# Optimization experiments

Hardware: AMD Instinct MI355X
Metric: run time of the kernel (lower is better)

Reference implementation:

```python
import jax, jax.numpy as jnp
import numpy as np

N, E, D = 50000, 800000, 64  # nodes, edges, feature dim (all feature dims must match, see module)
EPS = 1e-5


def _linear_params(key, fin, fout):
    k1, k2 = jax.random.split(key)
    s = 1.0 / np.sqrt(fin)
    W = jax.random.uniform(k1, (fout, fin), minval=-s, maxval=s, dtype=jnp.float32)
    b = jax.random.uniform(k2, (fout,), minval=-s, maxval=s, dtype=jnp.float32)
    return W, b


def setup_inputs() -> dict:
    key = jax.random.key(0)
    ks = jax.random.split(key, 9)
    h = jax.random.normal(ks[0], (N, D), dtype=jnp.float32)
    e = jax.random.normal(ks[1], (E, D), dtype=jnp.float32)
    src = jax.random.randint(ks[2], (E,), 0, N)
    dst = jax.random.randint(ks[3], (E,), 0, N)
    W_upd, b_upd = _linear_params(ks[4], 3 * D, D)   # upd_linear: cat(h_src,h_dst,e) -> D
    W_act, b_act = _linear_params(ks[5], D, D)       # activation_linear
    W_gd, b_gd = _linear_params(ks[6], D, D)         # gating_dst_linear
    W_gs, b_gs = _linear_params(ks[7], D, D)         # gating_src_linear
    W_out, b_out = _linear_params(ks[8], D, D)       # final linear
    g_un = jnp.ones((D,), jnp.float32); be_un = jnp.zeros((D,), jnp.float32)  # upd_norm gamma/beta
    g_gn = jnp.ones((D,), jnp.float32); be_gn = jnp.zeros((D,), jnp.float32)  # gating_norm gamma/beta
    return dict(h=h, e=e, src=src, dst=dst,
                W_upd=W_upd, b_upd=b_upd, g_un=g_un, be_un=be_un,
                W_act=W_act, b_act=b_act, W_gd=W_gd, b_gd=b_gd,
                W_gs=W_gs, b_gs=b_gs, g_gn=g_gn, be_gn=be_gn,
                W_out=W_out, b_out=b_out)


def _batchnorm(x, gamma, beta):
    # nn.BatchNorm1d in training mode: biased batch stats over axis 0
    m = x.mean(axis=0)
    v = x.var(axis=0)
    return (x - m) * jax.lax.rsqrt(v + EPS) * gamma + beta


def reference(h, e, src, dst, W_upd, b_upd, g_un, be_un, W_act, b_act,
              W_gd, b_gd, W_gs, b_gs, g_gn, be_gn, W_out, b_out):
    n_nodes = h.shape[0]
    # --- edge update: gather endpoints, linear, batchnorm, SiLU, residual ---
    e_cat = jnp.concatenate([h[src], h[dst], e], axis=1)       # [E, 3D]
    e_lin = e_cat @ W_upd.T + b_upd                             # [E, D]
    e2 = e + jax.nn.silu(_batchnorm(e_lin, g_un, be_un))        # residual (dims equal)
    # --- edge softmax grouped by destination node ---
    logit = e2 @ W_act.T + b_act                                # [E, D]
    mx = jax.ops.segment_max(logit, dst, num_segments=n_nodes)  # [N, D]
    ex = jnp.exp(logit - mx[dst])
    den = jax.ops.segment_sum(ex, dst, num_segments=n_nodes)
    a = ex / den[dst]                                           # [E, D]
    # --- gated aggregation: mail = a * W_gd h_dst, scatter-sum to dst ---
    mail = a * (h[dst] @ W_gd.T + b_gd)                         # [E, D]
    agg = jax.ops.segment_sum(mail, dst, num_segments=n_nodes)  # [N, D]
    h2 = (h @ W_gs.T + b_gs) + agg
    h2 = jax.nn.silu(_batchnorm(h2, g_gn, be_gn)) + h
    h2 = h2 @ W_out.T + b_out
    return (h2, e2)
```

## Files before the change

kernel.cpp:

```cpp
#include <hip/hip_runtime.h>

#define N_NODES 50000
#define N_EDGES 800000
#define EPS_BN 1e-5f


typedef __attribute__((ext_vector_type(8))) short s16x8;
typedef __attribute__((ext_vector_type(4))) float f32x4;

__device__ __forceinline__ unsigned short f2bf(float f) {
  unsigned int u = __float_as_uint(f);
  u += 0x7FFFu + ((u >> 16) & 1u);
  return (unsigned short)(u >> 16);
}
__device__ __forceinline__ unsigned int pack2(float lo, float hi) {
  return (unsigned int)f2bf(lo) | ((unsigned int)f2bf(hi) << 16);
}
__device__ __forceinline__ s16x8 cvt8(float4 a, float4 b) {
  union { s16x8 v; unsigned int u[4]; } r;
  r.u[0] = pack2(a.x, a.y); r.u[1] = pack2(a.z, a.w);
  r.u[2] = pack2(b.x, b.y); r.u[3] = pack2(b.z, b.w);
  return r.v;
}
__device__ __forceinline__ float siluf(float x) { return x / (1.f + __expf(-x)); }

__global__ void k_pre(unsigned int* __restrict__ wsu,
                      const float* __restrict__ W_upd, const float* __restrict__ W_gd,
                      const float* __restrict__ W_gs, const float* __restrict__ W_out,
                      const float* __restrict__ h, short* __restrict__ hbf) {
  int b = blockIdx.x;
  if (b < 49) {
    int i = b * 256 + threadIdx.x;
    if (i < 512) wsu[i] = 0u;
    if (i < 12500) wsu[12800 + i] = 0u;
    if (i < 6144) {
      int s = i >> 2, w = i & 3;
      int row = s / 24, slot = s - row * 24;
      int ii = slot ^ (row & 7);
      int fidx = row * 192 + ii * 8 + w * 2;
      wsu[512 + i] = pack2(W_upd[fidx], W_upd[fidx + 1]);
    }
    if (i < 2048) {
      float2 a = *(const float2*)&W_gd[(size_t)i * 2];
      float2 bb = *(const float2*)&W_gs[(size_t)i * 2];
      float2 c = *(const float2*)&W_out[(size_t)i * 2];
      wsu[6656 + i] = pack2(a.x, a.y);
      wsu[8704 + i] = pack2(bb.x, bb.y);
      wsu[10752 + i] = pack2(c.x, c.y);
    }
  } else {
    int t = (b - 49) * 256 + threadIdx.x;
    if (t < (N_NODES * 64) / 8) {
      float4 a = *(const float4*)&h[(size_t)t * 8];
      float4 bb = *(const float4*)&h[(size_t)t * 8 + 4];
      *(s16x8*)&hbf[(size_t)t * 8] = cvt8(a, bb);
    }
  }
}

template<int PHASE>
__global__ __launch_bounds__(256, PHASE == 0 ? 5 : 4) void k_edge(
    const short* __restrict__ hbf, const float* __restrict__ e,
    const int* __restrict__ src, const int* __restrict__ dst,
    const unsigned int* __restrict__ wsu, const float* __restrict__ b_upd,
    const float* __restrict__ ws, unsigned char* __restrict__ flb,
    float* __restrict__ out_e)
{
  __shared__ short Bls[64 * 192];
  __shared__ float red[4][128];

  int tid = threadIdx.x;
  int ln = tid & 63, wv = tid >> 6;
  int lr = ln & 15, lq = ln >> 4, lk = lq * 8;
  int m0 = blockIdx.x * 128;
  int r0 = wv * 32 + lr, r1 = r0 + 16;
  int mA = m0 + r0, mB = m0 + r1;

  const float* pe0 = e + (size_t)mA * 64 + lk;
  const float* pe1 = e + (size_t)mB * 64 + lk;
  float4 e0a = *(const float4*)(pe0);
  float4 e0b = *(const float4*)(pe0 + 4);
  float4 e0c = *(const float4*)(pe0 + 32);
  float4 e0d = *(const float4*)(pe0 + 36);
  float4 e1a = *(const float4*)(pe1);
  float4 e1b = *(const float4*)(pe1 + 4);
  float4 e1c = *(const float4*)(pe1 + 32);
  float4 e1d = *(const float4*)(pe1 + 36);

  int s0 = src[mA], d0 = dst[mA];
  int s1i = src[mB], d1 = dst[mB];

  if (PHASE == 0 && lq == 0) { flb[d0] = 1; flb[d1] = 1; }

  s16x8 A0[6], A1[6];
  A0[0] = *(const s16x8*)&hbf[s0 * 64 + lk];
  A0[1] = *(const s16x8*)&hbf[s0 * 64 + 32 + lk];
  A0[2] = *(const s16x8*)&hbf[d0 * 64 + lk];
  A0[3] = *(const s16x8*)&hbf[d0 * 64 + 32 + lk];
  A1[0] = *(const s16x8*)&hbf[s1i * 64 + lk];
  A1[1] = *(const s16x8*)&hbf[s1i * 64 + 32 + lk];
  A1[2] = *(const s16x8*)&hbf[d1 * 64 + lk];
  A1[3] = *(const s16x8*)&hbf[d1 * 64 + 32 + lk];

  {
    unsigned int* bls32 = (unsigned int*)Bls;
    #pragma unroll
    for (int j = 0; j < 6; ++j) {
      int base = (j * 4 + wv) * 256;
      __builtin_amdgcn_global_load_lds(
          (__attribute__((address_space(1))) void*)(unsigned int*)(wsu + 512 + base + ln * 4),
          (__attribute__((address_space(3))) void*)(bls32 + base),
          16, 0, 0);
    }
  }

  A0[4] = cvt8(e0a, e0b);
  A0[5] = cvt8(e0c, e0d);
  A1[4] = cvt8(e1a, e1b);
  A1[5] = cvt8(e1c, e1d);
  __syncthreads();

  int rl = ln >> 4, c0 = (ln & 15) * 4;
  float4 epre[2][4];
  if (PHASE == 1) {
    #pragma unroll
    for (int rt = 0; rt < 2; ++rt)
      #pragma unroll
      for (int q = 0; q < 4; ++q)
        epre[rt][q] = *(const float4*)&e[(size_t)(m0 + wv * 32 + rt * 16 + rl * 4 + q) * 64 + c0];
  }

  f32x4 zero4 = {0.f, 0.f, 0.f, 0.f};
  f32x4 acc[2][4];
  #pragma unroll
  for (int rt = 0; rt < 2; ++rt)
    #pragma unroll
    for (int ct = 0; ct < 4; ++ct) acc[rt][ct] = zero4;

  #pragma unroll
  for (int ct = 0; ct < 4; ++ct) {
    int row = ct * 16 + lr, r7 = row & 7;
    #pragma unroll
    for (int kk = 0; kk < 6; ++kk) {
      s16x8 b = *(const s16x8*)&Bls[row * 192 + (((kk * 4 + lq) ^ r7) << 3)];
      acc[0][ct] = __builtin_amdgcn_mfma_f32_16x16x32_bf16(A0[kk], b, acc[0][ct], 0, 0, 0);
      acc[1][ct] = __builtin_amdgcn_mfma_f32_16x16x32_bf16(A1[kk], b, acc[1][ct], 0, 0, 0);
    }
  }

  if (PHASE == 0) {
    float s1[4], s2[4];
    #pragma unroll
    for (int ct = 0; ct < 4; ++ct) {
      float bias = b_upd[ct * 16 + lr];
      float a1s = 0.f, a2s = 0.f;
      #pragma unroll
      for (int rt = 0; rt < 2; ++rt)
        #pragma unroll
        for (int q = 0; q < 4; ++q) {
          float v = acc[rt][ct][q] + bias;
          a1s += v; a2s += v * v;
        }
      s1[ct] = a1s; s2[ct] = a2s;
    }
    #pragma unroll
    for (int ct = 0; ct < 4; ++ct) {
      s1[ct] += __shfl_xor(s1[ct], 16); s1[ct] += __shfl_xor(s1[ct], 32);
      s2[ct] += __shfl_xor(s2[ct], 16); s2[ct] += __shfl_xor(s2[ct], 32);
    }
    if (ln < 16) {
      #pragma unroll
      for (int ct = 0; ct < 4; ++ct) {
        red[wv][ct * 16 + ln] = s1[ct];
        red[wv][64 + ct * 16 + ln] = s2[ct];
      }
    }
    __syncthreads();
    if (tid < 128) {
      float t = red[0][tid] + red[1][tid] + red[2][tid] + red[3][tid];
      out_e[(size_t)blockIdx.x * 128 + tid] = t;
    }
  } else {
    #pragma unroll
    for (int ct = 0; ct < 4; ++ct) {
      int col = ct * 16 + lr;
      float scale = ws[128 + col], shift = ws[192 + col], bias = b_upd[col];
      #pragma unroll
      for (int rt = 0; rt < 2; ++rt)
        #pragma unroll
        for (int q = 0; q < 4; ++q) {
          float x = acc[rt][ct][q] + bias;
          acc[rt][ct][q] = siluf(x * scale + shift);
        }
    }
    __syncthreads();
    float* T = (float*)((char*)Bls + wv * 1280);
    #pragma unroll
    for (int rt = 0; rt < 2; ++rt) {
      #pragma unroll
      for (int q = 0; q < 4; ++q) {
        #pragma unroll
        for (int ct = 0; ct < 4; ++ct)
          T[lq * 72 + ct * 16 + lr] = acc[rt][ct][q];
        float4 t4 = *(const float4*)&T[rl * 72 + c0];
        float4 ev = epre[rt][q];
        t4.x += ev.x; t4.y += ev.y; t4.z += ev.z; t4.w += ev.w;
        *(float4*)&out_e[(size_t)(m0 + wv * 32 + rt * 16 + rl * 4 + q) * 64 + c0] = t4;
      }
    }
  }
}

__global__ void k_redfin(const float* __restrict__ partials, float* __restrict__ ws,
                         const float* __restrict__ gamma, const float* __restrict__ beta,
                         float rcount) {
  __shared__ float sr[2][256];
  int c = blockIdx.x;
  float s1 = 0.f, s2 = 0.f;
  for (int i = threadIdx.x; i < N_EDGES / 128; i += 256) {
    s1 += partials[(size_t)i * 128 + c];
    s2 += partials[(size_t)i * 128 + 64 + c];
  }
  sr[0][threadIdx.x] = s1; sr[1][threadIdx.x] = s2;
  __syncthreads();
  for (int off = 128; off >= 1; off >>= 1) {
    if (threadIdx.x < off) {
      sr[0][threadIdx.x] += sr[0][threadIdx.x + off];
      sr[1][threadIdx.x] += sr[1][threadIdx.x + off];
    }
    __syncthreads();
  }
  if (threadIdx.x == 0) {
    float mean = sr[0][0] * rcount;
    float var = sr[1][0] * rcount - mean * mean;
    float a = rsqrtf(var + EPS_BN) * gamma[c];
    ws[128 + c] = a;
    ws[192 + c] = beta[c] - mean * a;
  }
}

__global__ void k_fin(float* __restrict__ ws, const float* __restrict__ gamma,
                      const float* __restrict__ beta, float rcount, int off) {
  int d = threadIdx.x;
  float mean = ws[off + d] * rcount;
  float var = ws[off + 64 + d] * rcount - mean * mean;
  float inv = rsqrtf(var + EPS_BN);
  float a = inv * gamma[d];
  ws[off + 128 + d] = a;
  ws[off + 192 + d] = beta[d] - mean * a;
}

__global__ __launch_bounds__(256, 4) void k_nstat(
    const short* __restrict__ hbf, const unsigned int* __restrict__ wsu,
    const unsigned char* __restrict__ flb,
    const float* __restrict__ b_gd, const float* __restrict__ b_gs,
    float* __restrict__ ws, float* __restrict__ v_out)
{
  __shared__ short Bgd[64 * 64], Bgs[64 * 64];
  __shared__ float red[4][128];
  int tid = threadIdx.x;
  int ln = tid & 63, wv = tid >> 6;
  int lr = ln & 15, lq = ln >> 4, lk = lq * 8;
  int n0 = blockIdx.x * 128;

  const uint4* Sgd = (const uint4*)(wsu + 6656);
  const uint4* Sgs = (const uint4*)(wsu + 8704);
  #pragma unroll
  for (int j = 0; j < 2; ++j) {
    int c = tid + j * 256;
    int row = c >> 3, i = c & 7, sl = row * 8 + (i ^ (row & 7));
    ((uint4*)Bgd)[sl] = Sgd[c];
    ((uint4*)Bgs)[sl] = Sgs[c];
  }

  int r0 = wv * 32 + lr, r1 = r0 + 16;
  int nA = min(n0 + r0, N_NODES - 1), nB = min(n0 + r1, N_NODES - 1);
  s16x8 A0[2], A1[2];
  A0[0] = *(const s16x8*)&hbf[nA * 64 + lk];
  A0[1] = *(const s16x8*)&hbf[nA * 64 + 32 + lk];
  A1[0] = *(const s16x8*)&hbf[nB * 64 + lk];
  A1[1] = *(const s16x8*)&hbf[nB * 64 + 32 + lk];
  __syncthreads();

  f32x4 zero4 = {0.f, 0.f, 0.f, 0.f};
  f32x4 accd[2][4], accs[2][4];
  #pragma unroll
  for (int rt = 0; rt < 2; ++rt)
    #pragma unroll
    for (int ct = 0; ct < 4; ++ct) { accd[rt][ct] = zero4; accs[rt][ct] = zero4; }

  #pragma unroll
  for (int ct = 0; ct < 4; ++ct) {
    int row = ct * 16 + lr, r7 = row & 7;
    #pragma unroll
    for (int kk = 0; kk < 2; ++kk) {
      int sl = ((kk * 4 + lq) ^ r7) << 3;
      s16x8 bd = *(const s16x8*)&Bgd[row * 64 + sl];
      s16x8 bs = *(const s16x8*)&Bgs[row * 64 + sl];
      accd[0][ct] = __builtin_amdgcn_mfma_f32_16x16x32_bf16(A0[kk], bd, accd[0][ct], 0, 0, 0);
      accd[1][ct] = __builtin_amdgcn_mfma_f32_16x16x32_bf16(A1[kk], bd, accd[1][ct], 0, 0, 0);
      accs[0][ct] = __builtin_amdgcn_mfma_f32_16x16x32_bf16(A0[kk], bs, accs[0][ct], 0, 0, 0);
      accs[1][ct] = __builtin_amdgcn_mfma_f32_16x16x32_bf16(A1[kk], bs, accs[1][ct], 0, 0, 0);
    }
  }

  float s1[4], s2[4];
  #pragma unroll
  for (int ct = 0; ct < 4; ++ct) {
    int col = ct * 16 + lr;
    float bd = b_gd[col], bs = b_gs[col];
    float a1s = 0.f, a2s = 0.f;
    #pragma unroll
    for (int rt = 0; rt < 2; ++rt)
      #pragma unroll
      for (int q = 0; q < 4; ++q) {
        int row = wv * 32 + rt * 16 + lq * 4 + q;
        int n = n0 + row;
        if (n < N_NODES) {
          float fl = (float)flb[n];
          float v = accs[rt][ct][q] + bs + fl * (accd[rt][ct][q] + bd);
          v_out[(size_t)n * 64 + col] = v;
          a1s += v; a2s += v * v;
        }
      }
    s1[ct] = a1s; s2[ct] = a2s;
  }
  #pragma unroll
  for (int ct = 0; ct < 4; ++ct) {
    s1[ct] += __shfl_xor(s1[ct], 16); s1[ct] += __shfl_xor(s1[ct], 32);
    s2[ct] += __shfl_xor(s2[ct], 16); s2[ct] += __shfl_xor(s2[ct], 32);
  }
  if (ln < 16) {
    #pragma unroll
    for (int ct = 0; ct < 4; ++ct) {
      red[wv][ct * 16 + ln] = s1[ct];
      red[wv][64 + ct * 16 + ln] = s2[ct];
    }
  }
  __syncthreads();
  if (tid < 128) {
    float t = red[0][tid] + red[1][tid] + red[2][tid] + red[3][tid];
    atomicAdd(&ws[256 + tid], t);
  }
}

__global__ __launch_bounds__(256, 4) void k_nout(
    const float* __restrict__ h, const unsigned int* __restrict__ wsu,
    const float* __restrict__ b_out, const float* __restrict__ ws,
    const float* __restrict__ v_in, float* __restrict__ out_h)
{
  __shared__ short R1[128 * 64];
  __shared__ short R2[64 * 64];
  int tid = threadIdx.x;
  int ln = tid & 63, wv = tid >> 6;
  int lr = ln & 15, lq = ln >> 4;
  int n0 = blockIdx.x * 128;

  const uint4* Sot = (const uint4*)(wsu + 10752);
  #pragma unroll
  for (int j = 0; j < 2; ++j) {
    int c = tid + j * 256;
    int row = c >> 3, i = c & 7, sl = row * 8 + (i ^ (row & 7));
    ((uint4*)R2)[sl] = Sot[c];
  }

  int c0 = (tid & 15) * 4;
  int rbase = tid >> 4;
  float4 scl = *(const float4*)&ws[384 + c0];
  float4 shf = *(const float4*)&ws[448 + c0];
  #pragma unroll
  for (int i = 0; i < 8; ++i) {
    int row = rbase + 16 * i;
    int n = min(n0 + row, N_NODES - 1);
    float4 v4 = *(const float4*)&v_in[(size_t)n * 64 + c0];
    float4 h4 = *(const float4*)&h[(size_t)n * 64 + c0];
    float tx = siluf(v4.x * scl.x + shf.x) + h4.x;
    float ty = siluf(v4.y * scl.y + shf.y) + h4.y;
    float tz = siluf(v4.z * scl.z + shf.z) + h4.z;
    float tw = siluf(v4.w * scl.w + shf.w) + h4.w;
    int sl = ((((c0 >> 3) ^ (row & 7)) << 3) | (c0 & 7));
    unsigned int* p = (unsigned int*)&R1[row * 64 + sl];
    p[0] = pack2(tx, ty);
    p[1] = pack2(tz, tw);
  }
  __syncthreads();

  int r0 = wv * 32 + lr, r1 = r0 + 16;
  s16x8 T0[2], T1[2];
  #pragma unroll
  for (int kk = 0; kk < 2; ++kk) {
    T0[kk] = *(const s16x8*)&R1[r0 * 64 + (((kk * 4 + lq) ^ (r0 & 7)) << 3)];
    T1[kk] = *(const s16x8*)&R1[r1 * 64 + (((kk * 4 + lq) ^ (r1 & 7)) << 3)];
  }
  f32x4 zero4 = {0.f, 0.f, 0.f, 0.f};
  f32x4 ac2[2][4];
  #pragma unroll
  for (int rt = 0; rt < 2; ++rt)
    #pragma unroll
    for (int ct = 0; ct < 4; ++ct) ac2[rt][ct] = zero4;
  #pragma unroll
  for (int ct = 0; ct < 4; ++ct) {
    int row = ct * 16 + lr, r7 = row & 7;
    #pragma unroll
    for (int kk = 0; kk < 2; ++kk) {
      s16x8 b = *(const s16x8*)&R2[row * 64 + (((kk * 4 + lq) ^ r7) << 3)];
      ac2[0][ct] = __builtin_amdgcn_mfma_f32_16x16x32_bf16(T0[kk], b, ac2[0][ct], 0, 0, 0);
      ac2[1][ct] = __builtin_amdgcn_mfma_f32_16x16x32_bf16(T1[kk], b, ac2[1][ct], 0, 0, 0);
    }
  }
  #pragma unroll
  for (int ct = 0; ct < 4; ++ct) {
    int col = ct * 16 + lr;
    float bo = b_out[col];
    #pragma unroll
    for (int rt = 0; rt < 2; ++rt)
      #pragma unroll
      for (int q = 0; q < 4; ++q) {
        int row = wv * 32 + rt * 16 + lq * 4 + q;
        int n = n0 + row;
        if (n < N_NODES) out_h[(size_t)n * 64 + col] = ac2[rt][ct][q] + bo;
      }
  }
}

extern "C" void kernel_launch(void* const* d_in, const int* in_sizes, int n_in,
                              void* d_out, int out_size, void* d_ws, size_t ws_size,
                              hipStream_t stream) {
  const float* h     = (const float*)d_in[0];
  const float* e     = (const float*)d_in[1];
  const int*   src   = (const int*)d_in[2];
  const int*   dst   = (const int*)d_in[3];
  const float* W_upd = (const float*)d_in[4];
  const float* b_upd = (const float*)d_in[5];
  const float* g_un  = (const float*)d_in[6];
  const float* be_un = (const float*)d_in[7];
  const float* W_gd  = (const float*)d_in[10];
  const float* b_gd  = (const float*)d_in[11];
  const float* W_gs  = (const float*)d_in[12];
  const float* b_gs  = (const float*)d_in[13];
  const float* g_gn  = (const float*)d_in[14];
  const float* be_gn = (const float*)d_in[15];
  const float* W_out = (const float*)d_in[16];
  const float* b_out = (const float*)d_in[17];

  float* outH = (float*)d_out;
  float* outE = outH + (size_t)N_NODES * 64;
  float* ws = (float*)d_ws;
  unsigned int* wsu = (unsigned int*)d_ws;
  unsigned char* flb = (unsigned char*)(wsu + 12800);
  short* hbf = (short*)(wsu + 25600);

  k_pre<<<49 + 1563, 256, 0, stream>>>(wsu, W_upd, W_gd, W_gs, W_out, h, hbf);
  k_edge<0><<<N_EDGES / 128, 256, 0, stream>>>(hbf, e, src, dst, wsu, b_upd, ws, flb, outH);
  k_redfin<<<64, 256, 0, stream>>>(outH, ws, g_un, be_un, 1.f / (float)N_EDGES);
  k_edge<1><<<N_EDGES / 128, 256, 0, stream>>>(hbf, e, src, dst, wsu, b_upd, ws, flb, outE);
  k_nstat<<<(N_NODES + 127) / 128, 256, 0, stream>>>(hbf, wsu, flb, b_gd, b_gs, ws, outH);
  k_fin<<<1, 64, 0, stream>>>(ws, g_gn, be_gn, 1.f / (float)N_NODES, 256);
  k_nout<<<(N_NODES + 127) / 128, 256, 0, stream>>>(h, wsu, b_out, ws, outH, outH);
}
```

Baseline: 241.7 us.

## Fuse node-stat kernel into edge phase-1 launch and fold BN finalize into output kernel

Appends the node-stat blocks (gating GEMMs, pre-norm value and batch-stat atomics) as extra blocks of the phase-1 edge kernel, so they run alongside the edge blocks instead of as a separate launch. The separate finalize kernel is removed: every output block recomputes the node batchnorm scale and shift from the accumulated sums into shared memory. This cuts two kernel launches and their serialization gaps. In exchange the node blocks inherit the edge kernel's launch bounds and shared-memory footprint, and the scale/shift math is repeated per block.

```diff
diff --git a/kernel.cpp b/kernel.cpp
--- a/kernel.cpp
+++ b/kernel.cpp
@@ -3,6 +3,8 @@
 #define N_NODES 50000
 #define N_EDGES 800000
 #define EPS_BN 1e-5f
+#define EBLK (N_EDGES / 128)
+#define NBLK ((N_NODES + 127) / 128)
 
 
 typedef __attribute__((ext_vector_type(8))) short s16x8;
@@ -64,6 +66,8 @@
     const int* __restrict__ src, const int* __restrict__ dst,
     const unsigned int* __restrict__ wsu, const float* __restrict__ b_upd,
     const float* __restrict__ ws, unsigned char* __restrict__ flb,
+    const float* __restrict__ b_gd, const float* __restrict__ b_gs,
+    float* __restrict__ wsm, float* __restrict__ v_out,
     float* __restrict__ out_e)
 {
   __shared__ short Bls[64 * 192];
@@ -72,6 +76,90 @@
   int tid = threadIdx.x;
   int ln = tid & 63, wv = tid >> 6;
   int lr = ln & 15, lq = ln >> 4, lk = lq * 8;
+
+  if (PHASE == 1 && blockIdx.x >= EBLK) {
+    short* Bgd = Bls;
+    short* Bgs = Bls + 4096;
+    const uint4* Sgd = (const uint4*)(wsu + 6656);
+    const uint4* Sgs = (const uint4*)(wsu + 8704);
+    #pragma unroll
+    for (int j = 0; j < 2; ++j) {
+      int c = tid + j * 256;
+      int row = c >> 3, i = c & 7, sl = row * 8 + (i ^ (row & 7));
+      ((uint4*)Bgd)[sl] = Sgd[c];
+      ((uint4*)Bgs)[sl] = Sgs[c];
+    }
+    int n0 = (blockIdx.x - EBLK) * 128;
+    int r0 = wv * 32 + lr, r1 = r0 + 16;
+    int nA = min(n0 + r0, N_NODES - 1), nB = min(n0 + r1, N_NODES - 1);
+    s16x8 A0[2], A1[2];
+    A0[0] = *(const s16x8*)&hbf[nA * 64 + lk];
+    A0[1] = *(const s16x8*)&hbf[nA * 64 + 32 + lk];
+    A1[0] = *(const s16x8*)&hbf[nB * 64 + lk];
+    A1[1] = *(const s16x8*)&hbf[nB * 64 + 32 + lk];
+    __syncthreads();
+
+    f32x4 zero4 = {0.f, 0.f, 0.f, 0.f};
+    f32x4 accd[2][4], accs[2][4];
+    #pragma unroll
+    for (int rt = 0; rt < 2; ++rt)
+      #pragma unroll
+      for (int ct = 0; ct < 4; ++ct) { accd[rt][ct] = zero4; accs[rt][ct] = zero4; }
+    #pragma unroll
+    for (int ct = 0; ct < 4; ++ct) {
+      int row = ct * 16 + lr, r7 = row & 7;
+      #pragma unroll
+      for (int kk = 0; kk < 2; ++kk) {
+        int sl = ((kk * 4 + lq) ^ r7) << 3;
+        s16x8 bd = *(const s16x8*)&Bgd[row * 64 + sl];
+        s16x8 bs = *(const s16x8*)&Bgs[row * 64 + sl];
+        accd[0][ct] = __builtin_amdgcn_mfma_f32_16x16x32_bf16(A0[kk], bd, accd[0][ct], 0, 0, 0);
+        accd[1][ct] = __builtin_amdgcn_mfma_f32_16x16x32_bf16(A1[kk], bd, accd[1][ct], 0, 0, 0);
+        accs[0][ct] = __builtin_amdgcn_mfma_f32_16x16x32_bf16(A0[kk], bs, accs[0][ct], 0, 0, 0);
+        accs[1][ct] = __builtin_amdgcn_mfma_f32_16x16x32_bf16(A1[kk], bs, accs[1][ct], 0, 0, 0);
+      }
+    }
+    float s1[4], s2[4];
+    #pragma unroll
+    for (int ct = 0; ct < 4; ++ct) {
+      int col = ct * 16 + lr;
+      float bd = b_gd[col], bs = b_gs[col];
+      float a1s = 0.f, a2s = 0.f;
+      #pragma unroll
+      for (int rt = 0; rt < 2; ++rt)
+        #pragma unroll
+        for (int q = 0; q < 4; ++q) {
+          int row = wv * 32 + rt * 16 + lq * 4 + q;
+          int n = n0 + row;
+          if (n < N_NODES) {
+            float fl = (float)flb[n];
+            float v = accs[rt][ct][q] + bs + fl * (accd[rt][ct][q] + bd);
+            v_out[(size_t)n * 64 + col] = v;
+            a1s += v; a2s += v * v;
+          }
+        }
+      s1[ct] = a1s; s2[ct] = a2s;
+    }
+    #pragma unroll
+    for (int ct = 0; ct < 4; ++ct) {
+      s1[ct] += __shfl_xor(s1[ct], 16); s1[ct] += __shfl_xor(s1[ct], 32);
+      s2[ct] += __shfl_xor(s2[ct], 16); s2[ct] += __shfl_xor(s2[ct], 32);
+    }
+    if (ln < 16) {
+      #pragma unroll
+      for (int ct = 0; ct < 4; ++ct) {
+        red[wv][ct * 16 + ln] = s1[ct];
+        red[wv][64 + ct * 16 + ln] = s2[ct];
+      }
+    }
+    __syncthreads();
+    if (tid < 128) {
+      float t = red[0][tid] + red[1][tid] + red[2][tid] + red[3][tid];
+      atomicAdd(&wsm[256 + tid], t);
+    }
+    return;
+  }
+
   int m0 = blockIdx.x * 128;
   int r0 = wv * 32 + lr, r1 = r0 + 16;
   int mA = m0 + r0, mB = m0 + r1;
@@ -217,7 +305,7 @@
   __shared__ float sr[2][256];
   int c = blockIdx.x;
   float s1 = 0.f, s2 = 0.f;
-  for (int i = threadIdx.x; i < N_EDGES / 128; i += 256) {
+  for (int i = threadIdx.x; i < EBLK; i += 256) {
     s1 += partials[(size_t)i * 128 + c];
     s2 += partials[(size_t)i * 128 + 64 + c];
   }
@@ -239,118 +327,15 @@
   }
 }
 
-__global__ void k_fin(float* __restrict__ ws, const float* __restrict__ gamma,
-                      const float* __restrict__ beta, float rcount, int off) {
-  int d = threadIdx.x;
-  float mean = ws[off + d] * rcount;
-  float var = ws[off + 64 + d] * rcount - mean * mean;
-  float inv = rsqrtf(var + EPS_BN);
-  float a = inv * gamma[d];
-  ws[off + 128 + d] = a;
-  ws[off + 192 + d] = beta[d] - mean * a;
-}
-
-__global__ __launch_bounds__(256, 4) void k_nstat(
-    const short* __restrict__ hbf, const unsigned int* __restrict__ wsu,
-    const unsigned char* __restrict__ flb,
-    const float* __restrict__ b_gd, const float* __restrict__ b_gs,
-    float* __restrict__ ws, float* __restrict__ v_out)
-{
-  __shared__ short Bgd[64 * 64], Bgs[64 * 64];
-  __shared__ float red[4][128];
-  int tid = threadIdx.x;
-  int ln = tid & 63, wv = tid >> 6;
-  int lr = ln & 15, lq = ln >> 4, lk = lq * 8;
-  int n0 = blockIdx.x * 128;
-
-  const uint4* Sgd = (const uint4*)(wsu + 6656);
-  const uint4* Sgs = (const uint4*)(wsu + 8704);
-  #pragma unroll
-  for (int j = 0; j < 2; ++j) {
-    int c = tid + j * 256;
-    int row = c >> 3, i = c & 7, sl = row * 8 + (i ^ (row & 7));
-    ((uint4*)Bgd)[sl] = Sgd[c];
-    ((uint4*)Bgs)[sl] = Sgs[c];
-  }
-
-  int r0 = wv * 32 + lr, r1 = r0 + 16;
-  int nA = min(n0 + r0, N_NODES - 1), nB = min(n0 + r1, N_NODES - 1);
-  s16x8 A0[2], A1[2];
-  A0[0] = *(const s16x8*)&hbf[nA * 64 + lk];
-  A0[1] = *(const s16x8*)&hbf[nA * 64 + 32 + lk];
-  A1[0] = *(const s16x8*)&hbf[nB * 64 + lk];
-  A1[1] = *(const s16x8*)&hbf[nB * 64 + 32 + lk];
-  __syncthreads();
-
-  f32x4 zero4 = {0.f, 0.f, 0.f, 0.f};
-  f32x4 accd[2][4], accs[2][4];
-  #pragma unroll
-  for (int rt = 0; rt < 2; ++rt)
-    #pragma unroll
-    for (int ct = 0; ct < 4; ++ct) { accd[rt][ct] = zero4; accs[rt][ct] = zero4; }
-
-  #pragma unroll
-  for (int ct = 0; ct < 4; ++ct) {
-    int row = ct * 16 + lr, r7 = row & 7;
-    #pragma unroll
-    for (int kk = 0; kk < 2; ++kk) {
-      int sl = ((kk * 4 + lq) ^ r7) << 3;
-      s16x8 bd = *(const s16x8*)&Bgd[row * 64 + sl];
-      s16x8 bs = *(const s16x8*)&Bgs[row * 64 + sl];
-      accd[0][ct] = __builtin_amdgcn_mfma_f32_16x16x32_bf16(A0[kk], bd, accd[0][ct], 0, 0, 0);
-      accd[1][ct] = __builtin_amdgcn_mfma_f32_16x16x32_bf16(A1[kk], bd, accd[1][ct], 0, 0, 0);
-      accs[0][ct] = __builtin_amdgcn_mfma_f32_16x16x32_bf16(A0[kk], bs, accs[0][ct], 0, 0, 0);
-      accs[1][ct] = __builtin_amdgcn_mfma_f32_16x16x32_bf16(A1[kk], bs, accs[1][ct], 0, 0, 0);
-    }
-  }
-
-  float s1[4], s2[4];
-  #pragma unroll
-  for (int ct = 0; ct < 4; ++ct) {
-    int col = ct * 16 + lr;
-    float bd = b_gd[col], bs = b_gs[col];
-    float a1s = 0.f, a2s = 0.f;
-    #pragma unroll
-    for (int rt = 0; rt < 2; ++rt)
-      #pragma unroll
-      for (int q = 0; q < 4; ++q) {
-        int row = wv * 32 + rt * 16 + lq * 4 + q;
-        int n = n0 + row;
-        if (n < N_NODES) {
-          float fl = (float)flb[n];
-          float v = accs[rt][ct][q] + bs + fl * (accd[rt][ct][q] + bd);
-          v_out[(size_t)n * 64 + col] = v;
-          a1s += v; a2s += v * v;
-        }
-      }
-    s1[ct] = a1s; s2[ct] = a2s;
-  }
-  #pragma unroll
-  for (int ct = 0; ct < 4; ++ct) {
-    s1[ct] += __shfl_xor(s1[ct], 16); s1[ct] += __shfl_xor(s1[ct], 32);
-    s2[ct] += __shfl_xor(s2[ct], 16); s2[ct] += __shfl_xor(s2[ct], 32);
-  }
-  if (ln < 16) {
-    #pragma unroll
-    for (int ct = 0; ct < 4; ++ct) {
-      red[wv][ct * 16 + ln] = s1[ct];
-      red[wv][64 + ct * 16 + ln] = s2[ct];
-    }
-  }
-  __syncthreads();
-  if (tid < 128) {
-    float t = red[0][tid] + red[1][tid] + red[2][tid] + red[3][tid];
-    atomicAdd(&ws[256 + tid], t);
-  }
-}
-
 __global__ __launch_bounds__(256, 4) void k_nout(
     const float* __restrict__ h, const unsigned int* __restrict__ wsu,
+    const float* __restrict__ g_gn, const float* __restrict__ be_gn,
     const float* __restrict__ b_out, const float* __restrict__ ws,
     const float* __restrict__ v_in, float* __restrict__ out_h)
 {
   __shared__ short R1[128 * 64];
   __shared__ short R2[64 * 64];
+  __shared__ float sA[64], sB[64];
   int tid = threadIdx.x;
   int ln = tid & 63, wv = tid >> 6;
   int lr = ln & 15, lq = ln >> 4;
@@ -363,11 +348,19 @@
     int row = c >> 3, i = c & 7, sl = row * 8 + (i ^ (row & 7));
     ((uint4*)R2)[sl] = Sot[c];
   }
+  if (tid < 64) {
+    float mean = ws[256 + tid] * (1.f / (float)N_NODES);
+    float var = ws[320 + tid] * (1.f / (float)N_NODES) - mean * mean;
+    float a = rsqrtf(var + EPS_BN) * g_gn[tid];
+    sA[tid] = a;
+    sB[tid] = be_gn[tid] - mean * a;
+  }
+  __syncthreads();
 
   int c0 = (tid & 15) * 4;
   int rbase = tid >> 4;
-  float4 scl = *(const float4*)&ws[384 + c0];
-  float4 shf = *(const float4*)&ws[448 + c0];
+  float4 scl = *(const float4*)&sA[c0];
+  float4 shf = *(const float4*)&sB[c0];
   #pragma unroll
   for (int i = 0; i < 8; ++i) {
     int row = rbase + 16 * i;
@@ -451,10 +444,10 @@
   short* hbf = (short*)(wsu + 25600);
 
   k_pre<<<49 + 1563, 256, 0, stream>>>(wsu, W_upd, W_gd, W_gs, W_out, h, hbf);
-  k_edge<0><<<N_EDGES / 128, 256, 0, stream>>>(hbf, e, src, dst, wsu, b_upd, ws, flb, outH);
+  k_edge<0><<<EBLK, 256, 0, stream>>>(hbf, e, src, dst, wsu, b_upd, ws, flb,
+                                      nullptr, nullptr, nullptr, nullptr, outH);
   k_redfin<<<64, 256, 0, stream>>>(outH, ws, g_un, be_un, 1.f / (float)N_EDGES);
-  k_edge<1><<<N_EDGES / 128, 256, 0, stream>>>(hbf, e, src, dst, wsu, b_upd, ws, flb, outE);
-  k_nstat<<<(N_NODES + 127) / 128, 256, 0, stream>>>(hbf, wsu, flb, b_gd, b_gs, ws, outH);
-  k_fin<<<1, 64, 0, stream>>>(ws, g_gn, be_gn, 1.f / (float)N_NODES, 256);
-  k_nout<<<(N_NODES + 127) / 128, 256, 0, stream>>>(h, wsu, b_out, ws, outH, outH);
-}
+  k_edge<1><<<EBLK + NBLK, 256, 0, stream>>>(hbf, e, src, dst, wsu, b_upd, ws, flb,
+                                             b_gd, b_gs, ws, outH, outE);
+  k_nout<<<NBLK, 256, 0, stream>>>(h, wsu, g_gn, be_gn, b_out, ws, outH, outH);
+}
```

Result: faster. 229.1 us, median of 2 (-5.2%).
